# Performance work log

Measured on AMD Instinct MI355X. Metric: run time of the kernel, lower is better.

## Reference

```python
import jax, jax.numpy as jnp
import numpy as np

B, S, D = 2, 2048, 2048
H, G = 16, 4
HD = D // H          # head_dim = 128
KV = HD * G          # 512


def setup_inputs() -> dict:
    key = jax.random.key(0)
    ks = jax.random.split(key, 5)
    scale = 1.0 / np.sqrt(D)
    return {
        "x": jax.random.normal(ks[0], (B, S, D), dtype=jnp.float32),
        "Wqkv": jax.random.normal(ks[1], (D, D + 2 * KV), dtype=jnp.float32) * scale,
        "bqkv": jax.random.normal(ks[2], (D + 2 * KV,), dtype=jnp.float32) * 0.01,
        "Wout": jax.random.normal(ks[3], (D, D), dtype=jnp.float32) * scale,
        "bout": jax.random.normal(ks[4], (D,), dtype=jnp.float32) * 0.01,
    }


def reference(x, Wqkv, bqkv, Wout, bout):
    b, s, _ = x.shape
    qkv = x @ Wqkv + bqkv                                  # [b, s, D + 2*KV]
    q, k, v = jnp.split(qkv, [D, D + KV], axis=-1)
    q = q.reshape(b, s, H, HD)                             # [b, s, H, hd]
    # torch .repeat tiles the group axis: head h -> group (h % G)
    k = jnp.tile(k.reshape(b, s, G, HD), (1, 1, H // G, 1))  # [b, s, H, hd]
    v = jnp.tile(v.reshape(b, s, G, HD), (1, 1, H // G, 1))
    # NOTE: original divides by head_dim (not sqrt(head_dim)) -- kept faithfully
    scores = jnp.einsum("bqhd,bkhd->bhqk", q, k) / HD      # [b, H, s, s]
    prob = jax.nn.softmax(scores, axis=-1)
    out = jnp.einsum("bhqk,bkhd->bqhd", prob, v).reshape(b, s, D)
    return out @ Wout + bout
```

## Files before the change

### kernel.cpp

```cpp
#include <hip/hip_runtime.h>
#include <stdint.h>

typedef __bf16 bf16;
typedef __bf16 bf16x8 __attribute__((ext_vector_type(8)));
typedef __bf16 bf16x4 __attribute__((ext_vector_type(4)));
typedef float  f32x4  __attribute__((ext_vector_type(4)));

#define B_   2
#define S_   2048
#define D_   2048
#define H_   16
#define G_   4
#define HD_  128
#define KV_  512
#define NQKV 3072
#define M_   4096

__device__ __forceinline__ void async16(bf16* lds, const bf16* g) {
  __builtin_amdgcn_global_load_lds(
      (const __attribute__((address_space(1))) unsigned int*)g,
      (__attribute__((address_space(3))) unsigned int*)lds, 16, 0, 0);
}

__device__ __forceinline__ f32x4 mfma16(bf16x8 a, bf16x8 b, f32x4 c) {
  return __builtin_amdgcn_mfma_f32_16x16x32_bf16(a, b, c, 0, 0, 0);
}

__global__ void convert_x_kernel(const float* __restrict__ in,
                                 bf16* __restrict__ out, int n4) {
  int i = blockIdx.x * blockDim.x + threadIdx.x;
  if (i >= n4) return;
  float4 v = ((const float4*)in)[i];
  bf16x4 o = { (bf16)v.x, (bf16)v.y, (bf16)v.z, (bf16)v.w };
  *(bf16x4*)(out + (size_t)i * 4) = o;
}

__global__ void transpose_w_kernel(const float* __restrict__ in,
                                   bf16* __restrict__ out,
                                   int rows, int cols) {
  __shared__ float tile[32][33];
  int bc = blockIdx.x * 32;
  int br = blockIdx.y * 32;
  int tx = threadIdx.x, ty = threadIdx.y;
  #pragma unroll
  for (int i = 0; i < 32; i += 8)
    tile[ty + i][tx] = in[(size_t)(br + ty + i) * cols + bc + tx];
  __syncthreads();
  #pragma unroll
  for (int i = 0; i < 32; i += 8)
    out[(size_t)(bc + ty + i) * rows + br + tx] = (bf16)tile[tx][ty + i];
}

__global__ void transpose_v_kernel(const bf16* __restrict__ qkv,
                                   bf16* __restrict__ vt) {
  __shared__ bf16 tile[32][33];
  int bg = blockIdx.z; int b = bg / G_, g = bg % G_;
  int sb = blockIdx.x * 32, db = blockIdx.y * 32;
  int tx = threadIdx.x, ty = threadIdx.y;
  const bf16* src = qkv + (size_t)b * S_ * NQKV + (D_ + KV_ + g * HD_);
  #pragma unroll
  for (int i = 0; i < 32; i += 8)
    tile[ty + i][tx] = src[(size_t)(sb + ty + i) * NQKV + db + tx];
  __syncthreads();
  bf16* dst = vt + (size_t)(b * G_ + g) * HD_ * S_;
  #pragma unroll
  for (int i = 0; i < 32; i += 8)
    dst[(size_t)(db + ty + i) * S_ + sb + tx] = tile[tx][ty + i];
}

template <int OUT_BF16>
__global__ __launch_bounds__(256) void gemm_bt(const bf16* __restrict__ A,
                                               const bf16* __restrict__ Bt,
                                               const float* __restrict__ bias,
                                               void* __restrict__ Cout,
                                               int Ndim, int K) {
  __shared__ __align__(16) bf16 As[128 * 32];
  __shared__ __align__(16) bf16 Bs[128 * 32];
  int t = threadIdx.x;
  int w = t >> 6, l = t & 63, lr = l & 15, lg = l >> 4;
  int wm = w >> 1, wn = w & 1;
  int row0 = blockIdx.x * 128, col0 = blockIdx.y * 128;

  f32x4 acc[4][4] = {};

  const bf16* ga = A  + (size_t)(row0 + (t >> 2)) * K + (t & 3) * 8;
  const bf16* gb = Bt + (size_t)(col0 + (t >> 2)) * K + (t & 3) * 8;

  for (int k0 = 0; k0 < K; k0 += 32) {
    __syncthreads();
    #pragma unroll
    for (int i = 0; i < 2; i++)
      async16(&As[w * 512 + i * 2048], ga + (size_t)i * 64 * K + k0);
    #pragma unroll
    for (int i = 0; i < 2; i++)
      async16(&Bs[w * 512 + i * 2048], gb + (size_t)i * 64 * K + k0);
    __syncthreads();

    bf16x8 af[4], bfr[4];
    #pragma unroll
    for (int mi = 0; mi < 4; mi++)
      af[mi] = *(const bf16x8*)&As[(wm * 64 + mi * 16 + lr) * 32 + lg * 8];
    #pragma unroll
    for (int ni = 0; ni < 4; ni++)
      bfr[ni] = *(const bf16x8*)&Bs[(wn * 64 + ni * 16 + lr) * 32 + lg * 8];
    #pragma unroll
    for (int mi = 0; mi < 4; mi++)
      #pragma unroll
      for (int ni = 0; ni < 4; ni++)
        acc[mi][ni] = mfma16(af[mi], bfr[ni], acc[mi][ni]);
  }

  float bv[4];
  #pragma unroll
  for (int ni = 0; ni < 4; ni++)
    bv[ni] = bias[col0 + wn * 64 + ni * 16 + lr];

  #pragma unroll
  for (int mi = 0; mi < 4; mi++)
    #pragma unroll
    for (int ni = 0; ni < 4; ni++)
      #pragma unroll
      for (int r = 0; r < 4; r++) {
        int row = row0 + wm * 64 + mi * 16 + lg * 4 + r;
        int col = col0 + wn * 64 + ni * 16 + lr;
        float v = acc[mi][ni][r] + bv[ni];
        if (OUT_BF16)
          ((bf16*)Cout)[(size_t)row * Ndim + col] = (bf16)v;
        else
          ((float*)Cout)[(size_t)row * Ndim + col] = v;
      }
}

__global__ __launch_bounds__(256, 2) void attn_kernel(const bf16* __restrict__ qkv,
                                                      const bf16* __restrict__ vt,
                                                      bf16* __restrict__ attnb) {
  __shared__ __align__(16) bf16 Ks[2][64 * 128];
  __shared__ __align__(16) bf16 Vs[2][128 * 64];
  __shared__ __align__(16) bf16 Ps[4][32 * 64];

  int t = threadIdx.x, w = t >> 6, l = t & 63, lr = l & 15, lg = l >> 4;
  int rsw = lr & 7;
  int lin = blockIdx.x + gridDim.x * blockIdx.y;
  int swz = (lin & 7) * 64 + (lin >> 3);
  int q0 = (swz & 15) * 128;
  int bh = swz >> 4, b = bh >> 4, h = bh & 15, g = h & 3;

  bf16x8 qf[2][4];
  #pragma unroll
  for (int mi = 0; mi < 2; mi++) {
    const bf16* qbase = qkv + (size_t)(b * S_ + q0 + w * 32 + mi * 16 + lr) * NQKV + h * HD_;
    #pragma unroll
    for (int kc = 0; kc < 4; kc++)
      qf[mi][kc] = *(const bf16x8*)(qbase + kc * 32 + lg * 8);
  }

  const bf16* kbase = qkv + (size_t)b * S_ * NQKV + D_ + g * HD_;
  const bf16* vbase = vt + (size_t)(b * G_ + g) * HD_ * S_;

  int krowi = w * 4 + (l >> 4);
  int ksw = (l & 15) ^ (krowi & 7);
  const bf16* kgl = kbase + (size_t)krowi * NQKV + ksw * 8;
  int vrowi = w * 8 + (l >> 3);
  int vsw = (l & 7) ^ ((l >> 3) & 7);
  const bf16* vgl = vbase + (size_t)vrowi * S_ + vsw * 8;

  auto STAGE_KV = [&](int nb, int kv0) {
    #pragma unroll
    for (int i = 0; i < 4; i++)
      async16(&Ks[nb][w * 512 + i * 2048], kgl + (size_t)(kv0 + i * 16) * NQKV);
    #pragma unroll
    for (int i = 0; i < 4; i++)
      async16(&Vs[nb][w * 512 + i * 2048], vgl + (size_t)(i * 32) * S_ + kv0);
  };

  float lsump[2] = {};
  f32x4 accO[2][8] = {};

  STAGE_KV(0, 0);

  for (int ti = 0; ti < S_ / 64; ++ti) {
    int cur = ti & 1;
    __syncthreads();
    if (ti + 1 < S_ / 64) STAGE_KV(cur ^ 1, (ti + 1) * 64);

    const bf16* ks = &Ks[cur][0];
    const bf16* vs = &Vs[cur][0];

    f32x4 sacc[2][4] = {};
    __builtin_amdgcn_s_setprio(1);
    #pragma unroll
    for (int fk = 0; fk < 4; fk++) {
      bf16x8 kf[4];
      #pragma unroll
      for (int kc = 0; kc < 4; kc++)
        kf[kc] = *(const bf16x8*)&ks[(fk * 16 + lr) * 128 + (((kc * 4 + lg) ^ rsw) * 8)];
      #pragma unroll
      for (int mi = 0; mi < 2; mi++)
        #pragma unroll
        for (int kc = 0; kc < 4; kc++)
          sacc[mi][fk] = mfma16(kf[kc], qf[mi][kc], sacc[mi][fk]);
    }
    __builtin_amdgcn_s_setprio(0);

    bf16* psw = &Ps[w][0];
    #pragma unroll
    for (int mi = 0; mi < 2; mi++)
      #pragma unroll
      for (int fk = 0; fk < 4; fk++) {
        float p0 = __expf(sacc[mi][fk][0] * 0.0078125f);
        float p1 = __expf(sacc[mi][fk][1] * 0.0078125f);
        float p2 = __expf(sacc[mi][fk][2] * 0.0078125f);
        float p3 = __expf(sacc[mi][fk][3] * 0.0078125f);
        lsump[mi] += (p0 + p1) + (p2 + p3);
        bf16x4 pk = { (bf16)p0, (bf16)p1, (bf16)p2, (bf16)p3 };
        *(bf16x4*)&psw[(mi * 16 + lr) * 64 +
                       (((fk * 2 + (lg >> 1)) ^ rsw) * 8) + (lg & 1) * 4] = pk;
      }

    bf16x8 pa[2][2];
    #pragma unroll
    for (int mi = 0; mi < 2; mi++)
      #pragma unroll
      for (int kk = 0; kk < 2; kk++)
        pa[mi][kk] = *(const bf16x8*)&psw[(mi * 16 + lr) * 64 + (((kk * 4 + lg) ^ rsw) * 8)];

    __builtin_amdgcn_s_setprio(1);
    #pragma unroll
    for (int fd = 0; fd < 8; fd++) {
      bf16x8 vfr[2];
      #pragma unroll
      for (int kk = 0; kk < 2; kk++)
        vfr[kk] = *(const bf16x8*)&vs[(fd * 16 + lr) * 64 + (((kk * 4 + lg) ^ rsw) * 8)];
      #pragma unroll
      for (int mi = 0; mi < 2; mi++)
        #pragma unroll
        for (int kk = 0; kk < 2; kk++)
          accO[mi][fd] = mfma16(pa[mi][kk], vfr[kk], accO[mi][fd]);
    }
    __builtin_amdgcn_s_setprio(0);
  }

  #pragma unroll
  for (int mi = 0; mi < 2; mi++) {
    float s = lsump[mi];
    s += __shfl_xor(s, 16);
    s += __shfl_xor(s, 32);
    float rls[4];
    #pragma unroll
    for (int r = 0; r < 4; r++) rls[r] = 1.f / __shfl(s, lg * 4 + r);
    bf16* obase = attnb + (size_t)(b * S_ + q0 + w * 32 + mi * 16) * D_ + h * HD_;
    #pragma unroll
    for (int r = 0; r < 4; r++)
      #pragma unroll
      for (int fd = 0; fd < 8; fd++)
        obase[(size_t)(lg * 4 + r) * D_ + fd * 16 + lr] =
            (bf16)(accO[mi][fd][r] * rls[r]);
  }
}

extern "C" void kernel_launch(void* const* d_in, const int* in_sizes, int n_in,
                              void* d_out, int out_size, void* d_ws, size_t ws_size,
                              hipStream_t stream) {
  const float* x    = (const float*)d_in[0];
  const float* Wqkv = (const float*)d_in[1];
  const float* bqkv = (const float*)d_in[2];
  const float* Wout = (const float*)d_in[3];
  const float* bout = (const float*)d_in[4];
  float* out = (float*)d_out;

  char* p = (char*)d_ws;
  bf16* xb    = (bf16*)p; p += (size_t)M_ * D_ * 2;
  bf16* wqkvT = (bf16*)p; p += (size_t)NQKV * D_ * 2;
  bf16* woutT = (bf16*)p; p += (size_t)D_ * D_ * 2;
  bf16* qkvb  = (bf16*)p; p += (size_t)M_ * NQKV * 2;
  bf16* vtb   = (bf16*)p; p += (size_t)B_ * G_ * HD_ * S_ * 2;
  bf16* attnb = (bf16*)p; p += (size_t)M_ * D_ * 2;

  convert_x_kernel<<<dim3(M_ * D_ / 4 / 256), dim3(256), 0, stream>>>(x, xb, M_ * D_ / 4);
  transpose_w_kernel<<<dim3(NQKV / 32, D_ / 32), dim3(32, 8), 0, stream>>>(Wqkv, wqkvT, D_, NQKV);
  transpose_w_kernel<<<dim3(D_ / 32, D_ / 32), dim3(32, 8), 0, stream>>>(Wout, woutT, D_, D_);

  gemm_bt<1><<<dim3(M_ / 128, NQKV / 128), dim3(256), 0, stream>>>(xb, wqkvT, bqkv, (void*)qkvb, NQKV, D_);

  transpose_v_kernel<<<dim3(S_ / 32, HD_ / 32, B_ * G_), dim3(32, 8), 0, stream>>>(qkvb, vtb);

  attn_kernel<<<dim3(S_ / 128, B_ * H_), dim3(256), 0, stream>>>(qkvb, vtb, attnb);

  gemm_bt<0><<<dim3(M_ / 128, D_ / 128), dim3(256), 0, stream>>>(attnb, woutT, bout, (void*)out, D_, D_);
}
```

Before: 220.1 us.

## Merge prep kernels, regroup attention heads by KV group, interleave exp with QK MFMAs

Folds the x conversion and the two weight transposes into one prep_kernel launch to cut launch overhead and idle tails between small kernels. Reorders the attention block-to-head mapping so that consecutively scheduled blocks share the same KV group, which should improve L2 reuse of K and V. Moves the exp/P-store into the per-fk QK loop so the score accumulators shrink from 8 to 2 vectors, lowering register pressure and allowing softmax work to overlap with MFMAs. The merged prep kernel branches on block index and wastes one LDS tile on the conversion path.

```diff
diff --git a/kernel.cpp b/kernel.cpp
--- a/kernel.cpp
+++ b/kernel.cpp
@@ -26,29 +26,38 @@
   return __builtin_amdgcn_mfma_f32_16x16x32_bf16(a, b, c, 0, 0, 0);
 }
 
-__global__ void convert_x_kernel(const float* __restrict__ in,
-                                 bf16* __restrict__ out, int n4) {
-  int i = blockIdx.x * blockDim.x + threadIdx.x;
-  if (i >= n4) return;
-  float4 v = ((const float4*)in)[i];
-  bf16x4 o = { (bf16)v.x, (bf16)v.y, (bf16)v.z, (bf16)v.w };
-  *(bf16x4*)(out + (size_t)i * 4) = o;
-}
-
-__global__ void transpose_w_kernel(const float* __restrict__ in,
-                                   bf16* __restrict__ out,
-                                   int rows, int cols) {
+__global__ __launch_bounds__(256) void prep_kernel(const float* __restrict__ x,
+                                                   const float* __restrict__ Wqkv,
+                                                   const float* __restrict__ Wout,
+                                                   bf16* __restrict__ xb,
+                                                   bf16* __restrict__ wqkvT,
+                                                   bf16* __restrict__ woutT) {
   __shared__ float tile[32][33];
-  int bc = blockIdx.x * 32;
-  int br = blockIdx.y * 32;
-  int tx = threadIdx.x, ty = threadIdx.y;
-  #pragma unroll
-  for (int i = 0; i < 32; i += 8)
-    tile[ty + i][tx] = in[(size_t)(br + ty + i) * cols + bc + tx];
+  int bid = blockIdx.x;
+  int t = threadIdx.x;
+
+  if (bid < 8192) {
+    int i = bid * 256 + t;
+    float4 v = ((const float4*)x)[i];
+    bf16x4 o = { (bf16)v.x, (bf16)v.y, (bf16)v.z, (bf16)v.w };
+    *(bf16x4*)(xb + (size_t)i * 4) = o;
+    return;
+  }
+  bid -= 8192;
+
+  const float* src; bf16* dst; int rows, cols, nct;
+  if (bid < 6144) { src = Wqkv; dst = wqkvT; rows = 2048; cols = 3072; nct = 96; }
+  else { bid -= 6144; src = Wout; dst = woutT; rows = 2048; cols = 2048; nct = 64; }
+
+  int bc = (bid % nct) * 32, br = (bid / nct) * 32;
+  int tx = t & 31, ty = t >> 5;
+  #pragma unroll
+  for (int i = 0; i < 32; i += 8)
+    tile[ty + i][tx] = src[(size_t)(br + ty + i) * cols + bc + tx];
   __syncthreads();
   #pragma unroll
   for (int i = 0; i < 32; i += 8)
-    out[(size_t)(bc + ty + i) * rows + br + tx] = (bf16)tile[tx][ty + i];
+    dst[(size_t)(bc + ty + i) * rows + br + tx] = (bf16)tile[tx][ty + i];
 }
 
 __global__ void transpose_v_kernel(const bf16* __restrict__ qkv,
@@ -143,7 +152,9 @@
   int lin = blockIdx.x + gridDim.x * blockIdx.y;
   int swz = (lin & 7) * 64 + (lin >> 3);
   int q0 = (swz & 15) * 128;
-  int bh = swz >> 4, b = bh >> 4, h = bh & 15, g = h & 3;
+  int hb2 = swz >> 4;
+  int b = hb2 >> 4, gh = hb2 & 15;
+  int g = gh >> 2, h = (gh & 3) * 4 + g;
 
   bf16x8 qf[2][4];
   #pragma unroll
@@ -180,13 +191,14 @@
 
   for (int ti = 0; ti < S_ / 64; ++ti) {
     int cur = ti & 1;
+    int kv0 = ti * 64;
     __syncthreads();
-    if (ti + 1 < S_ / 64) STAGE_KV(cur ^ 1, (ti + 1) * 64);
+    if (ti + 1 < S_ / 64) STAGE_KV(cur ^ 1, kv0 + 64);
 
     const bf16* ks = &Ks[cur][0];
     const bf16* vs = &Vs[cur][0];
-
-    f32x4 sacc[2][4] = {};
+    bf16* psw = &Ps[w][0];
+
     __builtin_amdgcn_s_setprio(1);
     #pragma unroll
     for (int fk = 0; fk < 4; fk++) {
@@ -194,28 +206,25 @@
       #pragma unroll
       for (int kc = 0; kc < 4; kc++)
         kf[kc] = *(const bf16x8*)&ks[(fk * 16 + lr) * 128 + (((kc * 4 + lg) ^ rsw) * 8)];
+      f32x4 sacc[2] = {};
       #pragma unroll
       for (int mi = 0; mi < 2; mi++)
         #pragma unroll
         for (int kc = 0; kc < 4; kc++)
-          sacc[mi][fk] = mfma16(kf[kc], qf[mi][kc], sacc[mi][fk]);
-    }
-    __builtin_amdgcn_s_setprio(0);
-
-    bf16* psw = &Ps[w][0];
-    #pragma unroll
-    for (int mi = 0; mi < 2; mi++)
-      #pragma unroll
-      for (int fk = 0; fk < 4; fk++) {
-        float p0 = __expf(sacc[mi][fk][0] * 0.0078125f);
-        float p1 = __expf(sacc[mi][fk][1] * 0.0078125f);
-        float p2 = __expf(sacc[mi][fk][2] * 0.0078125f);
-        float p3 = __expf(sacc[mi][fk][3] * 0.0078125f);
+          sacc[mi] = mfma16(kf[kc], qf[mi][kc], sacc[mi]);
+      #pragma unroll
+      for (int mi = 0; mi < 2; mi++) {
+        float p0 = __expf(sacc[mi][0] * 0.0078125f);
+        float p1 = __expf(sacc[mi][1] * 0.0078125f);
+        float p2 = __expf(sacc[mi][2] * 0.0078125f);
+        float p3 = __expf(sacc[mi][3] * 0.0078125f);
         lsump[mi] += (p0 + p1) + (p2 + p3);
         bf16x4 pk = { (bf16)p0, (bf16)p1, (bf16)p2, (bf16)p3 };
         *(bf16x4*)&psw[(mi * 16 + lr) * 64 +
                        (((fk * 2 + (lg >> 1)) ^ rsw) * 8) + (lg & 1) * 4] = pk;
       }
+    }
+    __builtin_amdgcn_s_setprio(0);
 
     bf16x8 pa[2][2];
     #pragma unroll
@@ -276,9 +285,8 @@
   bf16* vtb   = (bf16*)p; p += (size_t)B_ * G_ * HD_ * S_ * 2;
   bf16* attnb = (bf16*)p; p += (size_t)M_ * D_ * 2;
 
-  convert_x_kernel<<<dim3(M_ * D_ / 4 / 256), dim3(256), 0, stream>>>(x, xb, M_ * D_ / 4);
-  transpose_w_kernel<<<dim3(NQKV / 32, D_ / 32), dim3(32, 8), 0, stream>>>(Wqkv, wqkvT, D_, NQKV);
-  transpose_w_kernel<<<dim3(D_ / 32, D_ / 32), dim3(32, 8), 0, stream>>>(Wout, woutT, D_, D_);
+  prep_kernel<<<dim3(8192 + 6144 + 4096), dim3(256), 0, stream>>>(
+      x, Wqkv, Wout, xb, wqkvT, woutT);
 
   gemm_bt<1><<<dim3(M_ / 128, NQKV / 128), dim3(256), 0, stream>>>(xb, wqkvT, bqkv, (void*)qkvb, NQKV, D_);
 
```

New measurement: 217.9 us. No clear change (-1.0%).
